# Kernel tuning notes

Measured on AMD Instinct MI355X. Metric: run time of the kernel, lower is better.

The kernel has to match this reference:

```python
import jax, jax.numpy as jnp
import numpy as np

N = 50000
E = 1600000
D_IN = 128
D_OUT = 128


def setup_inputs() -> dict:
    key = jax.random.key(0)
    k1, k2, k3, k4 = jax.random.split(key, 4)
    x = jax.random.normal(k1, (N, D_IN), dtype=jnp.float32)
    edge_index = jax.random.randint(k2, (2, E), 0, N, dtype=jnp.int64)
    # Linear(in_channels, out_channels) params (torch layout: W [out, in])
    bound = 1.0 / np.sqrt(D_IN)
    W = jax.random.uniform(k3, (D_OUT, D_IN), minval=-bound, maxval=bound, dtype=jnp.float32)
    b = jax.random.uniform(k4, (D_OUT,), minval=-bound, maxval=bound, dtype=jnp.float32)
    return {"x": x, "edge_index": edge_index, "W": W, "b": b}


def reference(x, edge_index, W, b):
    src, dst = edge_index[0], edge_index[1]
    # degree of each node as a source: tg.utils.degree(edge_index[0])
    deg = jax.ops.segment_sum(jnp.ones((E,), dtype=x.dtype), src, num_segments=N)
    norm = jnp.sqrt(deg + 1.0)[:, None]  # [N, 1]
    xn = x / norm
    # message passing with self_loop=True: scatter-add into x itself (out=x)
    agg = xn + jax.ops.segment_sum(xn[src], dst, num_segments=N)  # [N, D_IN]
    h = agg / norm
    return h @ W.T + b
```

## Files before the change

kernel.cpp:

```cpp
#include <hip/hip_runtime.h>

#define NN 50000
#define NE 1600000
#define D 128
#define RPB 40
#define NRS 4
#define RNG 12500
#define NC 32
#define CHUNK_S 50000
#define NC2 64
#define CHUNK_D 25000
#define CAP 67

#define WS_INV  0
#define WS_CNT  204800
#define WS_WT   256000
#define WS_PDST 321536
#define WS_PSRC 3521536
#define WS_XNB  321536
#define WS_CSR  13121536

__global__ __launch_bounds__(1024) void fused_pre(const int* __restrict__ ei,
                                                  const float* __restrict__ W,
                                                  unsigned char* __restrict__ psrc,
                                                  unsigned char* __restrict__ pdst,
                                                  float* __restrict__ Wt) {
    __shared__ int h[RNG];
    int bid = blockIdx.x;
    if (bid < 128) {
        int r = bid >> 5;
        int lo = r * RNG;
        for (int j = threadIdx.x; j < RNG; j += 1024) h[j] = 0;
        __syncthreads();
        const int* s = ei + (bid & 31) * CHUNK_S;
        for (int i = threadIdx.x; i < CHUNK_S; i += 1024) {
            int k = s[i] - lo;
            if ((unsigned)k < RNG) atomicAdd(&h[k], 1);
        }
        __syncthreads();
        unsigned char* p = psrc + (size_t)bid * RNG;
        for (int j = threadIdx.x; j < RNG; j += 1024) p[j] = (unsigned char)h[j];
    } else if (bid < 384) {
        int b2 = bid - 128;
        int r = b2 >> 6;
        int lo = r * RNG;
        for (int j = threadIdx.x; j < RNG; j += 1024) h[j] = 0;
        __syncthreads();
        const int* d = ei + NE + (b2 & 63) * CHUNK_D;
        for (int i = threadIdx.x; i < CHUNK_D; i += 1024) {
            int k = d[i] - lo;
            if ((unsigned)k < RNG) atomicAdd(&h[k], 1);
        }
        __syncthreads();
        unsigned char* p = pdst + (size_t)b2 * RNG;
        for (int j = threadIdx.x; j < RNG; j += 1024) p[j] = (unsigned char)h[j];
    } else {
        int i = (bid - 384) * 1024 + threadIdx.x;
        Wt[(i & 127) * D + (i >> 7)] = W[i];
    }
}

__global__ void reduce_bases(const unsigned char* __restrict__ psrc,
                             unsigned char* __restrict__ pdst,
                             float* __restrict__ inv,
                             unsigned char* __restrict__ cnt) {
    int k = blockIdx.x * blockDim.x + threadIdx.x;
    if (k >= NN) return;
    int r = k / RNG, j = k - r * RNG;
    size_t bs = (size_t)(r * NC) * RNG + j;
    int s = 0;
#pragma unroll 8
    for (int c = 0; c < NC; ++c) s += psrc[bs + (size_t)c * RNG];
    inv[k] = rsqrtf((float)s + 1.0f);
    size_t bd = (size_t)(r * NC2) * RNG + j;
    int run = 0;
#pragma unroll 8
    for (int c = 0; c < NC2; ++c) {
        size_t p = bd + (size_t)c * RNG;
        int v = pdst[p];
        pdst[p] = (unsigned char)run;
        run += v;
    }
    cnt[k] = (unsigned char)(run < 255 ? run : 255);
}

__global__ __launch_bounds__(1024) void fill_sorted(const int* __restrict__ ei,
                                                    const unsigned char* __restrict__ rel,
                                                    unsigned short* __restrict__ csr) {
    __shared__ int cur[RNG];
    int R = blockIdx.x >> 6, c = blockIdx.x & 63;
    int lo = R * RNG;
    const unsigned char* rslice = rel + (size_t)blockIdx.x * RNG;
    for (int j = threadIdx.x; j < RNG; j += 1024)
        cur[j] = (lo + j) * CAP + (int)rslice[j];
    __syncthreads();
    const int* s = ei + c * CHUNK_D;
    const int* d = ei + NE + c * CHUNK_D;
    for (int i = threadIdx.x; i < CHUNK_D; i += 1024) {
        int dv = d[i];
        int kd = dv - lo;
        if ((unsigned)kd < RNG) {
            int pos = atomicAdd(&cur[kd], 1);
            if (pos < (dv + 1) * CAP)
                csr[pos] = (unsigned short)s[i];
        }
    }
}

__device__ __forceinline__ unsigned bf16_rne(float f) {
    unsigned u = __float_as_uint(f);
    return (u + 0x7fffu + ((u >> 16) & 1u)) >> 16;
}
__global__ void scale_kernel(const float* __restrict__ x, const float* __restrict__ inv,
                             unsigned* __restrict__ xnb4) {
    int i = blockIdx.x * blockDim.x + threadIdx.x;
    if (i >= NN * 16) return;
    int row = i >> 4;
    float w = inv[row];
    const float4* src = (const float4*)(x + (size_t)i * 8);
    float4 a = src[0], bq = src[1];
    uint4 o;
    o.x = bf16_rne(a.x * w)  | (bf16_rne(a.y * w) << 16);
    o.y = bf16_rne(a.z * w)  | (bf16_rne(a.w * w) << 16);
    o.z = bf16_rne(bq.x * w) | (bf16_rne(bq.y * w) << 16);
    o.w = bf16_rne(bq.z * w) | (bf16_rne(bq.w * w) << 16);
    ((uint4*)xnb4)[i] = o;
}

#define ACC2(u) do { \
    ax += __uint_as_float((u).x << 16); \
    ay += __uint_as_float((u).x & 0xffff0000u); \
    az += __uint_as_float((u).y << 16); \
    aw += __uint_as_float((u).y & 0xffff0000u); } while (0)

__global__ __launch_bounds__(256) void gather_kernel(const unsigned* __restrict__ xnb,
                                                     const float* __restrict__ inv,
                                                     const unsigned char* __restrict__ cnt,
                                                     const unsigned short* __restrict__ csr,
                                                     float* __restrict__ out) {
    int wid = (blockIdx.x * blockDim.x + threadIdx.x) >> 6;
    if (wid >= NN) return;
    int lane = threadIdx.x & 63;
    int half = lane >> 5;
    int col4 = lane & 31;

    float ax = 0.f, ay = 0.f, az = 0.f, aw = 0.f;
    const uint2* xb = (const uint2*)xnb;
    if (half == 0) {
        uint2 u = xb[(size_t)wid * 32 + col4];
        ACC2(u);
    }
    int n = cnt[wid];
    const unsigned short* row = csr + (size_t)wid * CAP;
    int i = half;
    for (; i + 14 < n; i += 16) {
        int s0 = row[i],      s1 = row[i + 2],  s2 = row[i + 4],  s3 = row[i + 6];
        int s4 = row[i + 8],  s5 = row[i + 10], s6 = row[i + 12], s7 = row[i + 14];
        uint2 u0 = xb[(size_t)s0 * 32 + col4];
        uint2 u1 = xb[(size_t)s1 * 32 + col4];
        uint2 u2 = xb[(size_t)s2 * 32 + col4];
        uint2 u3 = xb[(size_t)s3 * 32 + col4];
        uint2 u4 = xb[(size_t)s4 * 32 + col4];
        uint2 u5 = xb[(size_t)s5 * 32 + col4];
        uint2 u6 = xb[(size_t)s6 * 32 + col4];
        uint2 u7 = xb[(size_t)s7 * 32 + col4];
        ACC2(u0); ACC2(u1); ACC2(u2); ACC2(u3);
        ACC2(u4); ACC2(u5); ACC2(u6); ACC2(u7);
    }
    for (; i + 6 < n; i += 8) {
        int s0 = row[i], s1 = row[i + 2], s2 = row[i + 4], s3 = row[i + 6];
        uint2 u0 = xb[(size_t)s0 * 32 + col4];
        uint2 u1 = xb[(size_t)s1 * 32 + col4];
        uint2 u2 = xb[(size_t)s2 * 32 + col4];
        uint2 u3 = xb[(size_t)s3 * 32 + col4];
        ACC2(u0); ACC2(u1); ACC2(u2); ACC2(u3);
    }
    for (; i < n; i += 2) {
        int s = row[i];
        uint2 u = xb[(size_t)s * 32 + col4];
        ACC2(u);
    }
    ax += __shfl_xor(ax, 32, 64);
    ay += __shfl_xor(ay, 32, 64);
    az += __shfl_xor(az, 32, 64);
    aw += __shfl_xor(aw, 32, 64);
    if (half == 0) {
        float wn = inv[wid];
        float4 o;
        o.x = ax * wn; o.y = ay * wn; o.z = az * wn; o.w = aw * wn;
        ((float4*)(out + (size_t)wid * D))[col4] = o;
    }
}

__global__ __launch_bounds__(256) void gemm_kernel(float* io, const float* __restrict__ Wt,
                                                   const float* __restrict__ b) {
    __shared__ float h[RPB][D];
    int r0 = blockIdx.x * RPB;

    const float4* src4 = (const float4*)(io + (size_t)r0 * D);
    for (int t = threadIdx.x; t < RPB * D / 4; t += 256) {
        ((float4*)h)[t] = src4[t];
    }
    __syncthreads();

    int c = threadIdx.x & 127;
    int rh = threadIdx.x >> 7;
    float acc[20];
#pragma unroll
    for (int j = 0; j < 20; ++j) acc[j] = 0.0f;

    for (int k0 = 0; k0 < D; k0 += 4) {
        float w0 = Wt[(k0 + 0) * D + c];
        float w1 = Wt[(k0 + 1) * D + c];
        float w2 = Wt[(k0 + 2) * D + c];
        float w3 = Wt[(k0 + 3) * D + c];
#pragma unroll
        for (int j = 0; j < 20; ++j) {
            float4 hv = *(const float4*)&h[rh * 20 + j][k0];
            acc[j] += hv.x * w0 + hv.y * w1 + hv.z * w2 + hv.w * w3;
        }
    }

    float bc = b[c];
#pragma unroll
    for (int j = 0; j < 20; ++j) {
        io[(size_t)(r0 + rh * 20 + j) * D + c] = acc[j] + bc;
    }
}

extern "C" void kernel_launch(void* const* d_in, const int* in_sizes, int n_in,
                              void* d_out, int out_size, void* d_ws, size_t ws_size,
                              hipStream_t stream) {
    const float* x  = (const float*)d_in[0];
    const int*   ei = (const int*)d_in[1];
    const float* W  = (const float*)d_in[2];
    const float* b  = (const float*)d_in[3];
    float* out = (float*)d_out;

    char* ws = (char*)d_ws;
    float*          inv  = (float*)         (ws + WS_INV);
    unsigned char*  cnt  = (unsigned char*) (ws + WS_CNT);
    float*          Wt   = (float*)         (ws + WS_WT);
    unsigned char*  pdst = (unsigned char*) (ws + WS_PDST);
    unsigned char*  psrc = (unsigned char*) (ws + WS_PSRC);
    unsigned*       xnb  = (unsigned*)      (ws + WS_XNB);
    unsigned short* csr  = (unsigned short*)(ws + WS_CSR);

    fused_pre<<<400, 1024, 0, stream>>>(ei, W, psrc, pdst, Wt);
    reduce_bases<<<(NN + 255) / 256, 256, 0, stream>>>(psrc, pdst, inv, cnt);
    fill_sorted<<<NRS * NC2, 1024, 0, stream>>>(ei, pdst, csr);
    scale_kernel<<<(NN * 16 + 255) / 256, 256, 0, stream>>>(x, inv, xnb);
    gather_kernel<<<(NN * 64 + 255) / 256, 256, 0, stream>>>(xnb, inv, cnt, csr, out);
    gemm_kernel<<<NN / RPB, 256, 0, stream>>>(out, Wt, b);
}
```

Before: 154.7 us.

## Pack histogram counters into 16-bit LDS words, widen ranges, register-tile GEMM

The histogram and fill kernels now keep two 16-bit counters per 32-bit LDS word. This lets each block cover 25000 nodes instead of 12500, with twice as many chunks per range, so there are fewer range passes over the edge list. The reduction loops grow to 64 and 128 chunk partials. The GEMM now gives each thread a 5x4 register tile with float4 weight loads and stores, and the CSR index and x loads use nontemporal hints. The cost is longer serial prefix loops in reduce_bases, and the packed 8-bit bucket counts in the 16-bit stores could overflow.

```diff
diff --git a/kernel.cpp b/kernel.cpp
--- a/kernel.cpp
+++ b/kernel.cpp
@@ -4,19 +4,19 @@
 #define NE 1600000
 #define D 128
 #define RPB 40
-#define NRS 4
-#define RNG 12500
-#define NC 32
-#define CHUNK_S 50000
-#define NC2 64
-#define CHUNK_D 25000
+#define RNG 25000
+#define CH_S 25000
+#define CH_D 12500
 #define CAP 67
+
+typedef float fvec4 __attribute__((ext_vector_type(4)));
+typedef unsigned uvec4 __attribute__((ext_vector_type(4)));
 
 #define WS_INV  0
 #define WS_CNT  204800
 #define WS_WT   256000
 #define WS_PDST 321536
-#define WS_PSRC 3521536
+#define WS_PSRC 6721536
 #define WS_XNB  321536
 #define WS_CSR  13121536
 
@@ -25,35 +25,39 @@
                                                   unsigned char* __restrict__ psrc,
                                                   unsigned char* __restrict__ pdst,
                                                   float* __restrict__ Wt) {
-    __shared__ int h[RNG];
+    __shared__ unsigned hw[RNG / 2];
     int bid = blockIdx.x;
     if (bid < 128) {
-        int r = bid >> 5;
-        int lo = r * RNG;
-        for (int j = threadIdx.x; j < RNG; j += 1024) h[j] = 0;
-        __syncthreads();
-        const int* s = ei + (bid & 31) * CHUNK_S;
-        for (int i = threadIdx.x; i < CHUNK_S; i += 1024) {
+        int lo = (bid >> 6) * RNG;
+        for (int j = threadIdx.x; j < RNG / 2; j += 1024) hw[j] = 0;
+        __syncthreads();
+        const int* s = ei + (bid & 63) * CH_S;
+        for (int i = threadIdx.x; i < CH_S; i += 1024) {
             int k = s[i] - lo;
-            if ((unsigned)k < RNG) atomicAdd(&h[k], 1);
-        }
-        __syncthreads();
-        unsigned char* p = psrc + (size_t)bid * RNG;
-        for (int j = threadIdx.x; j < RNG; j += 1024) p[j] = (unsigned char)h[j];
+            if ((unsigned)k < RNG) atomicAdd(&hw[k >> 1], 1u << ((k & 1) << 4));
+        }
+        __syncthreads();
+        unsigned short* p = (unsigned short*)(psrc + (size_t)bid * RNG);
+        for (int jw = threadIdx.x; jw < RNG / 2; jw += 1024) {
+            unsigned v = hw[jw];
+            p[jw] = (unsigned short)((v & 0xffu) | ((v >> 16) << 8));
+        }
     } else if (bid < 384) {
         int b2 = bid - 128;
-        int r = b2 >> 6;
-        int lo = r * RNG;
-        for (int j = threadIdx.x; j < RNG; j += 1024) h[j] = 0;
-        __syncthreads();
-        const int* d = ei + NE + (b2 & 63) * CHUNK_D;
-        for (int i = threadIdx.x; i < CHUNK_D; i += 1024) {
+        int lo = (b2 >> 7) * RNG;
+        for (int j = threadIdx.x; j < RNG / 2; j += 1024) hw[j] = 0;
+        __syncthreads();
+        const int* d = ei + NE + (b2 & 127) * CH_D;
+        for (int i = threadIdx.x; i < CH_D; i += 1024) {
             int k = d[i] - lo;
-            if ((unsigned)k < RNG) atomicAdd(&h[k], 1);
-        }
-        __syncthreads();
-        unsigned char* p = pdst + (size_t)b2 * RNG;
-        for (int j = threadIdx.x; j < RNG; j += 1024) p[j] = (unsigned char)h[j];
+            if ((unsigned)k < RNG) atomicAdd(&hw[k >> 1], 1u << ((k & 1) << 4));
+        }
+        __syncthreads();
+        unsigned short* p = (unsigned short*)(pdst + (size_t)b2 * RNG);
+        for (int jw = threadIdx.x; jw < RNG / 2; jw += 1024) {
+            unsigned v = hw[jw];
+            p[jw] = (unsigned short)((v & 0xffu) | ((v >> 16) << 8));
+        }
     } else {
         int i = (bid - 384) * 1024 + threadIdx.x;
         Wt[(i & 127) * D + (i >> 7)] = W[i];
@@ -66,16 +70,17 @@
                              unsigned char* __restrict__ cnt) {
     int k = blockIdx.x * blockDim.x + threadIdx.x;
     if (k >= NN) return;
-    int r = k / RNG, j = k - r * RNG;
-    size_t bs = (size_t)(r * NC) * RNG + j;
+    int r = k >= RNG;
+    int j = k - r * RNG;
+    size_t bs = (size_t)(r * 64) * RNG + j;
     int s = 0;
 #pragma unroll 8
-    for (int c = 0; c < NC; ++c) s += psrc[bs + (size_t)c * RNG];
+    for (int c = 0; c < 64; ++c) s += psrc[bs + (size_t)c * RNG];
     inv[k] = rsqrtf((float)s + 1.0f);
-    size_t bd = (size_t)(r * NC2) * RNG + j;
+    size_t bd = (size_t)(r * 128) * RNG + j;
     int run = 0;
 #pragma unroll 8
-    for (int c = 0; c < NC2; ++c) {
+    for (int c = 0; c < 128; ++c) {
         size_t p = bd + (size_t)c * RNG;
         int v = pdst[p];
         pdst[p] = (unsigned char)run;
@@ -84,47 +89,60 @@
     cnt[k] = (unsigned char)(run < 255 ? run : 255);
 }
 
+__device__ __forceinline__ unsigned bf16_rne(float f) {
+    unsigned u = __float_as_uint(f);
+    return (u + 0x7fffu + ((u >> 16) & 1u)) >> 16;
+}
+
+__device__ __forceinline__ void scale_one(const float* __restrict__ x,
+                                          const float* __restrict__ inv,
+                                          unsigned* __restrict__ xnb4, int i) {
+    int row = i >> 4;
+    float w = inv[row];
+    const fvec4* src = (const fvec4*)(x + (size_t)i * 8);
+    fvec4 a = __builtin_nontemporal_load(src);
+    fvec4 bq = __builtin_nontemporal_load(src + 1);
+    uvec4 o;
+    o.x = bf16_rne(a.x * w)  | (bf16_rne(a.y * w) << 16);
+    o.y = bf16_rne(a.z * w)  | (bf16_rne(a.w * w) << 16);
+    o.z = bf16_rne(bq.x * w) | (bf16_rne(bq.y * w) << 16);
+    o.w = bf16_rne(bq.z * w) | (bf16_rne(bq.w * w) << 16);
+    ((uvec4*)xnb4)[i] = o;
+}
+
 __global__ __launch_bounds__(1024) void fill_sorted(const int* __restrict__ ei,
                                                     const unsigned char* __restrict__ rel,
                                                     unsigned short* __restrict__ csr) {
-    __shared__ int cur[RNG];
-    int R = blockIdx.x >> 6, c = blockIdx.x & 63;
-    int lo = R * RNG;
-    const unsigned char* rslice = rel + (size_t)blockIdx.x * RNG;
-    for (int j = threadIdx.x; j < RNG; j += 1024)
-        cur[j] = (lo + j) * CAP + (int)rslice[j];
+    __shared__ unsigned cur[RNG / 2];
+    int bid = blockIdx.x;
+    int lo = (bid >> 7) * RNG;
+    int c = bid & 127;
+    const unsigned short* rslice = (const unsigned short*)(rel + (size_t)bid * RNG);
+    for (int jw = threadIdx.x; jw < RNG / 2; jw += 1024) {
+        unsigned w = rslice[jw];
+        cur[jw] = (w & 0xffu) | ((w >> 8) << 16);
+    }
     __syncthreads();
-    const int* s = ei + c * CHUNK_D;
-    const int* d = ei + NE + c * CHUNK_D;
-    for (int i = threadIdx.x; i < CHUNK_D; i += 1024) {
+    const int* s = ei + c * CH_D;
+    const int* d = ei + NE + c * CH_D;
+    for (int i = threadIdx.x; i < CH_D; i += 1024) {
         int dv = d[i];
         int kd = dv - lo;
         if ((unsigned)kd < RNG) {
-            int pos = atomicAdd(&cur[kd], 1);
-            if (pos < (dv + 1) * CAP)
-                csr[pos] = (unsigned short)s[i];
-        }
-    }
-}
-
-__device__ __forceinline__ unsigned bf16_rne(float f) {
-    unsigned u = __float_as_uint(f);
-    return (u + 0x7fffu + ((u >> 16) & 1u)) >> 16;
-}
+            int sh = (kd & 1) << 4;
+            unsigned old = atomicAdd(&cur[kd >> 1], 1u << sh);
+            int r2 = (old >> sh) & 0xffff;
+            if (r2 < CAP)
+                csr[(size_t)dv * CAP + r2] = (unsigned short)s[i];
+        }
+    }
+}
+
 __global__ void scale_kernel(const float* __restrict__ x, const float* __restrict__ inv,
                              unsigned* __restrict__ xnb4) {
     int i = blockIdx.x * blockDim.x + threadIdx.x;
     if (i >= NN * 16) return;
-    int row = i >> 4;
-    float w = inv[row];
-    const float4* src = (const float4*)(x + (size_t)i * 8);
-    float4 a = src[0], bq = src[1];
-    uint4 o;
-    o.x = bf16_rne(a.x * w)  | (bf16_rne(a.y * w) << 16);
-    o.y = bf16_rne(a.z * w)  | (bf16_rne(a.w * w) << 16);
-    o.z = bf16_rne(bq.x * w) | (bf16_rne(bq.y * w) << 16);
-    o.w = bf16_rne(bq.z * w) | (bf16_rne(bq.w * w) << 16);
-    ((uint4*)xnb4)[i] = o;
+    scale_one(x, inv, xnb4, i);
 }
 
 #define ACC2(u) do { \
@@ -154,8 +172,14 @@
     const unsigned short* row = csr + (size_t)wid * CAP;
     int i = half;
     for (; i + 14 < n; i += 16) {
-        int s0 = row[i],      s1 = row[i + 2],  s2 = row[i + 4],  s3 = row[i + 6];
-        int s4 = row[i + 8],  s5 = row[i + 10], s6 = row[i + 12], s7 = row[i + 14];
+        int s0 = __builtin_nontemporal_load(row + i);
+        int s1 = __builtin_nontemporal_load(row + i + 2);
+        int s2 = __builtin_nontemporal_load(row + i + 4);
+        int s3 = __builtin_nontemporal_load(row + i + 6);
+        int s4 = __builtin_nontemporal_load(row + i + 8);
+        int s5 = __builtin_nontemporal_load(row + i + 10);
+        int s6 = __builtin_nontemporal_load(row + i + 12);
+        int s7 = __builtin_nontemporal_load(row + i + 14);
         uint2 u0 = xb[(size_t)s0 * 32 + col4];
         uint2 u1 = xb[(size_t)s1 * 32 + col4];
         uint2 u2 = xb[(size_t)s2 * 32 + col4];
@@ -203,28 +227,38 @@
     }
     __syncthreads();
 
-    int c = threadIdx.x & 127;
-    int rh = threadIdx.x >> 7;
-    float acc[20];
-#pragma unroll
-    for (int j = 0; j < 20; ++j) acc[j] = 0.0f;
+    int c4 = (threadIdx.x & 31) * 4;
+    int rg = threadIdx.x >> 5;
+    float acc[5][4];
+#pragma unroll
+    for (int j = 0; j < 5; ++j)
+#pragma unroll
+        for (int cc = 0; cc < 4; ++cc) acc[j][cc] = 0.0f;
 
     for (int k0 = 0; k0 < D; k0 += 4) {
-        float w0 = Wt[(k0 + 0) * D + c];
-        float w1 = Wt[(k0 + 1) * D + c];
-        float w2 = Wt[(k0 + 2) * D + c];
-        float w3 = Wt[(k0 + 3) * D + c];
-#pragma unroll
-        for (int j = 0; j < 20; ++j) {
-            float4 hv = *(const float4*)&h[rh * 20 + j][k0];
-            acc[j] += hv.x * w0 + hv.y * w1 + hv.z * w2 + hv.w * w3;
-        }
-    }
-
-    float bc = b[c];
-#pragma unroll
-    for (int j = 0; j < 20; ++j) {
-        io[(size_t)(r0 + rh * 20 + j) * D + c] = acc[j] + bc;
+        float4 w0 = *(const float4*)&Wt[(k0 + 0) * D + c4];
+        float4 w1 = *(const float4*)&Wt[(k0 + 1) * D + c4];
+        float4 w2 = *(const float4*)&Wt[(k0 + 2) * D + c4];
+        float4 w3 = *(const float4*)&Wt[(k0 + 3) * D + c4];
+#pragma unroll
+        for (int j = 0; j < 5; ++j) {
+            float4 hv = *(const float4*)&h[rg * 5 + j][k0];
+            acc[j][0] += hv.x * w0.x + hv.y * w1.x + hv.z * w2.x + hv.w * w3.x;
+            acc[j][1] += hv.x * w0.y + hv.y * w1.y + hv.z * w2.y + hv.w * w3.y;
+            acc[j][2] += hv.x * w0.z + hv.y * w1.z + hv.z * w2.z + hv.w * w3.z;
+            acc[j][3] += hv.x * w0.w + hv.y * w1.w + hv.z * w2.w + hv.w * w3.w;
+        }
+    }
+
+    float4 bb = *(const float4*)&b[c4];
+#pragma unroll
+    for (int j = 0; j < 5; ++j) {
+        float4 o;
+        o.x = acc[j][0] + bb.x;
+        o.y = acc[j][1] + bb.y;
+        o.z = acc[j][2] + bb.z;
+        o.w = acc[j][3] + bb.w;
+        *(float4*)&io[(size_t)(r0 + rg * 5 + j) * D + c4] = o;
     }
 }
 
@@ -236,8 +270,8 @@
     const float* W  = (const float*)d_in[2];
     const float* b  = (const float*)d_in[3];
     float* out = (float*)d_out;
-
     char* ws = (char*)d_ws;
+
     float*          inv  = (float*)         (ws + WS_INV);
     unsigned char*  cnt  = (unsigned char*) (ws + WS_CNT);
     float*          Wt   = (float*)         (ws + WS_WT);
@@ -248,7 +282,7 @@
 
     fused_pre<<<400, 1024, 0, stream>>>(ei, W, psrc, pdst, Wt);
     reduce_bases<<<(NN + 255) / 256, 256, 0, stream>>>(psrc, pdst, inv, cnt);
-    fill_sorted<<<NRS * NC2, 1024, 0, stream>>>(ei, pdst, csr);
+    fill_sorted<<<256, 1024, 0, stream>>>(ei, pdst, csr);
     scale_kernel<<<(NN * 16 + 255) / 256, 256, 0, stream>>>(x, inv, xnb);
     gather_kernel<<<(NN * 64 + 255) / 256, 256, 0, stream>>>(xnb, inv, cnt, csr, out);
     gemm_kernel<<<NN / RPB, 256, 0, stream>>>(out, Wt, b);
```

After: 148.6 us. 1.04x faster.
